# Optimization experiments

Measured on AMD Instinct MI355X. Metric: run time of the kernel, lower is better.

The kernel has to match this reference:

```python
import jax, jax.numpy as jnp
import numpy as np

B, N, F = 4, 4096, 32
NG = 14  # number of gate graph-convs in GCNLSTM_Cell with memory state


def setup_inputs() -> dict:
    key = jax.random.key(0)
    ks = jax.random.split(key, 7)
    x = jax.random.normal(ks[0], (B, N, F), jnp.float32)
    h = jax.random.normal(ks[1], (B, N, F), jnp.float32)
    c = jax.random.normal(ks[2], (B, N, F), jnp.float32)
    m = jax.random.normal(ks[3], (B, N, F), jnp.float32)
    # weighted dense adjacency, scaled so row sums are O(1)
    adj = jax.random.uniform(ks[4], (N, N), jnp.float32) / N
    # 14 WeightedGraphConv layers: Dense F -> 2F (single FeedForward layer, no relu)
    W = jax.random.normal(ks[5], (NG, F, 2 * F), jnp.float32) * (1.0 / np.sqrt(F))
    b = jnp.zeros((NG, 2 * F), jnp.float32)
    return {"x": x, "h": h, "c": c, "m": m, "adj": adj, "W": W, "b": b}


def _gcn(ax, W, b):
    # ax: [B,N,F] = adj @ state (precomputed); Dense to 2F then GLU split.
    z = ax @ W + b  # [B,N,2F]
    ls, rs = jnp.split(z, 2, axis=-1)
    return ls * jax.nn.sigmoid(rs)


def reference(x, h, c, m, adj, W, b):
    # shared graph aggregation for x and h (adj is the same for all gates)
    ax = jnp.einsum('nm,bmf->bnf', adj, x)  # [B,N,F]
    ah = jnp.einsum('nm,bmf->bnf', adj, h)

    fx = _gcn(ax, W[0], b[0]); fh = _gcn(ah, W[1], b[1])
    ix = _gcn(ax, W[2], b[2]); ih = _gcn(ah, W[3], b[3])
    cx = _gcn(ax, W[4], b[4]); ch = _gcn(ah, W[5], b[5])
    ox = _gcn(ax, W[6], b[6]); oh = _gcn(ah, W[7], b[7])

    f = jax.nn.sigmoid(fx + fh)
    i = jax.nn.sigmoid(ix + ih)
    o = jax.nn.sigmoid(ox + oh)
    c_new = f * c + i * jnp.tanh(cx + ch)
    h1 = o * jnp.tanh(c_new)

    # memory-state block (6 more graph convs on h1 and m)
    ah1 = jnp.einsum('nm,bmf->bnf', adj, h1)
    am = jnp.einsum('nm,bmf->bnf', adj, m)
    sa_ih = _gcn(ah1, W[8], b[8]);  sa_im = _gcn(am, W[9], b[9])
    sa_gh = _gcn(ah1, W[10], b[10]); sa_gm = _gcn(am, W[11], b[11])
    sa_oh = _gcn(ah1, W[12], b[12]); sa_om = _gcn(am, W[13], b[13])

    i2 = jax.nn.sigmoid(sa_ih + sa_im)
    g = jax.nn.sigmoid(sa_gh + sa_gm)
    o2 = jax.nn.sigmoid(sa_oh + sa_om)
    m_new = i2 * m + (1.0 - i2) * g
    h_new = m_new * o2
    return h_new, c_new, m_new
```

## Files before the change

### kernel.cpp

```cpp
#include <hip/hip_runtime.h>
#include <stdint.h>

typedef __attribute__((ext_vector_type(4))) float f32x4;
typedef __attribute__((ext_vector_type(8))) short s16x8;

#define BB 4
#define NN 4096
#define FF 32
#define BNF (BB*NN*FF)

typedef __attribute__((address_space(3))) void       as3_void;
typedef const __attribute__((address_space(1))) void as1_cvoid;

static __device__ __forceinline__ float bf2f(uint16_t u) {
    union { uint32_t i; float f; } v; v.i = ((uint32_t)u) << 16; return v.f;
}
static __device__ __forceinline__ uint16_t f2bf(float f) {
    union { float f; uint32_t i; } v; v.f = f;
    uint32_t r = v.i + 0x7FFFu + ((v.i >> 16) & 1u);
    return (uint16_t)(r >> 16);
}
static __device__ __forceinline__ float sig_acc(float x) { return 1.0f / (1.0f + expf(-x)); }

__global__ __launch_bounds__(256) void prep_kernel(
    const float* __restrict__ adj, uint16_t* __restrict__ adjb, int cvtN,
    const float* __restrict__ Wf, uint16_t* __restrict__ Wp,
    const float* __restrict__ x, const float* __restrict__ h,
    const float* __restrict__ m,
    uint16_t* __restrict__ P, uint16_t* __restrict__ P2)
{
    int bid = blockIdx.x;
    int t = threadIdx.x;

    if (bid < cvtN) {
        size_t i = ((size_t)bid * 256 + t) * 8;
        float4 v0 = *(const float4*)(adj + i);
        float4 v1 = *(const float4*)(adj + i + 4);
        union { uint4 u; uint16_t e[8]; } o;
        o.e[0] = f2bf(v0.x); o.e[1] = f2bf(v0.y); o.e[2] = f2bf(v0.z); o.e[3] = f2bf(v0.w);
        o.e[4] = f2bf(v1.x); o.e[5] = f2bf(v1.y); o.e[6] = f2bf(v1.z); o.e[7] = f2bf(v1.w);
        *(uint4*)(adjb + i) = o.u;
        return;
    }
    bid -= cvtN;

    if (bid < 112) {
        int idx = bid * 256 + t;
        int g   = idx >> 11;
        int k   = (idx >> 6) & 31;
        int col = idx & 63;
        uint16_t v = f2bf(Wf[idx]);
        int gp = g >> 1;
        int sl = ((g & 1) << 2) | (k >> 3);
        int ph = sl ^ (col & 7);
        Wp[((gp * 64 + col) * 64) + ph * 8 + (k & 7)] = v;
        return;
    }
    bid -= 112;

    const float* src; uint16_t* dst; int rowbase, b, n0;
    if (bid < 512) {
        int tensor = bid >> 8;
        src = tensor ? h : x; dst = P; rowbase = tensor * 128;
        b = (bid >> 6) & 3; n0 = (bid & 63) * 64;
    } else {
        int q = bid - 512;
        src = m; dst = P2; rowbase = 128;
        b = q >> 6; n0 = (q & 63) * 64;
    }
    __shared__ uint16_t tl[32][65];
    {
        int i = t >> 2, ch = t & 3;
        size_t idx = ((size_t)(b * NN + n0 + i)) * FF + ch * 8;
        float4 v0 = *(const float4*)(src + idx);
        float4 v1 = *(const float4*)(src + idx + 4);
        uint16_t e[8] = { f2bf(v0.x), f2bf(v0.y), f2bf(v0.z), f2bf(v0.w),
                          f2bf(v1.x), f2bf(v1.y), f2bf(v1.z), f2bf(v1.w) };
        #pragma unroll
        for (int k = 0; k < 8; k++) tl[ch * 8 + k][i] = e[k];
    }
    __syncthreads();
    {
        int f = t >> 3, ch = t & 7;
        union { uint4 u; uint16_t e[8]; } v;
        #pragma unroll
        for (int k = 0; k < 8; k++) v.e[k] = tl[f][ch * 8 + k];
        size_t row = (size_t)(rowbase + b * 32 + f);
        *(uint4*)(dst + row * NN + n0 + ch * 8) = v.u;
    }
}

__global__ __launch_bounds__(256) void gemm_kernel(
    const void* __restrict__ Av,
    const uint16_t* __restrict__ Bt,
    float* __restrict__ part, uint16_t* __restrict__ Cb,
    int kLen, int direct, int isf32A)
{
    int mt = blockIdx.x, nt = blockIdx.y, ks = blockIdx.z;
    int m0 = mt * 128, c0 = nt * 128, k0 = ks * kLen;
    __shared__ __align__(16) uint16_t aL[128 * 32];
    __shared__ __align__(16) uint16_t bL[128 * 32];
    int t = threadIdx.x;
    int lane = t & 63, w = t >> 6;
    int wm = (w & 1) * 64, wn = (w >> 1) * 64;
    int lm = lane & 15, lk = lane >> 4;

    const uint16_t* A16 = (const uint16_t*)Av;
    const float*    Af  = (const float*)Av;

    f32x4 acc[4][4] = {};

    for (int kk = k0; kk < k0 + kLen; kk += 32) {
        if (!isf32A) {
            #pragma unroll
            for (int q = 0; q < 2; q++) {
                int pos  = q * 4096 + t * 16;
                int row  = pos >> 6;
                int slot = ((pos >> 4) & 3) ^ ((row >> 1) & 3);
                int col  = slot * 8;
                size_t aidx = (size_t)(m0 + row) * 4096 + kk + col;
                size_t bidx = (size_t)(c0 + row) * 4096 + kk + col;
                __builtin_amdgcn_global_load_lds((as1_cvoid*)(A16 + aidx),
                                                 (as3_void*)((char*)aL + pos), 16, 0, 0);
                __builtin_amdgcn_global_load_lds((as1_cvoid*)(Bt + bidx),
                                                 (as3_void*)((char*)bL + pos), 16, 0, 0);
            }
        } else {
            union { uint4 u; uint16_t e[8]; } sa[2], sb[2];
            #pragma unroll
            for (int q = 0; q < 2; q++) {
                int pos  = q * 4096 + t * 16;
                int row  = pos >> 6;
                int slot = ((pos >> 4) & 3) ^ ((row >> 1) & 3);
                int col  = slot * 8;
                size_t aidx = (size_t)(m0 + row) * 4096 + kk + col;
                size_t bidx = (size_t)(c0 + row) * 4096 + kk + col;
                union { uint4 u[2]; float f[8]; } va;
                va.u[0] = *(const uint4*)(Af + aidx);
                va.u[1] = *(const uint4*)(Af + aidx + 4);
                #pragma unroll
                for (int k = 0; k < 8; k++) sa[q].e[k] = f2bf(va.f[k]);
                sb[q].u = *(const uint4*)(Bt + bidx);
            }
            #pragma unroll
            for (int q = 0; q < 2; q++) {
                int pos = q * 4096 + t * 16;
                *(uint4*)((char*)aL + pos) = sa[q].u;
                *(uint4*)((char*)bL + pos) = sb[q].u;
            }
        }
        __syncthreads();
        s16x8 af[4], bfr[4];
        #pragma unroll
        for (int i = 0; i < 4; i++) {
            int r = wm + i * 16 + lm;
            af[i] = *(const s16x8*)(aL + r * 32 + ((lk ^ ((r >> 1) & 3)) * 8));
        }
        #pragma unroll
        for (int j = 0; j < 4; j++) {
            int r = wn + j * 16 + lm;
            bfr[j] = *(const s16x8*)(bL + r * 32 + ((lk ^ ((r >> 1) & 3)) * 8));
        }
        #pragma unroll
        for (int i = 0; i < 4; i++)
            #pragma unroll
            for (int j = 0; j < 4; j++)
                acc[i][j] = __builtin_amdgcn_mfma_f32_16x16x32_bf16(af[i], bfr[j], acc[i][j], 0, 0, 0);
        __syncthreads();
    }

    int r4 = (lane >> 4) * 4;
    if (direct) {
        #pragma unroll
        for (int i = 0; i < 4; i++)
            #pragma unroll
            for (int j = 0; j < 4; j++) {
                int c = c0 + wn + j * 16 + lm;
                int mr = m0 + wm + i * 16 + r4;
                union { uint2 u; uint16_t e[4]; } v;
                #pragma unroll
                for (int r = 0; r < 4; r++) v.e[r] = f2bf(acc[i][j][r]);
                *(uint2*)(Cb + (size_t)c * 4096 + mr) = v.u;
            }
    } else {
        #pragma unroll
        for (int i = 0; i < 4; i++)
            #pragma unroll
            for (int j = 0; j < 4; j++) {
                int c = c0 + wn + j * 16 + lm;
                int mr = m0 + wm + i * 16 + r4;
                *(f32x4*)(part + ((size_t)ks * 256 + c) * 4096 + mr) = acc[i][j];
            }
    }
}

__global__ __launch_bounds__(256) void fuse1_kernel(
    const float* __restrict__ part,
    const uint16_t* __restrict__ Cbi,
    const uint16_t* __restrict__ Wp,
    const float* __restrict__ bf_,
    const float* __restrict__ cf,
    float* __restrict__ cnew, uint16_t* __restrict__ S2t, int ns)
{
    __shared__ float    AL[64 * 17];
    __shared__ float    SX[4][64][9];
    __shared__ uint16_t H1[32 * 18];

    int t = threadIdx.x;
    int bid = blockIdx.x;
    int b = bid >> 8, n0 = (bid & 255) * 16;
    int lane = t & 63, w = t >> 6;
    int j = lane & 15, kg = lane >> 4;
    int ej = t & 15, erow = (t >> 4) & 15;

    float cv[2];
    #pragma unroll
    for (int hh = 0; hh < 2; hh++)
        cv[hh] = cf[((size_t)(b * NN + n0 + erow)) * FF + ej + hh * 16];

    {
        int r = t >> 2, ch = t & 3;
        int crow = (r < 32) ? (b * 32 + r) : (128 + b * 32 + (r - 32));
        if (ns) {
            const float* gp = part + (size_t)crow * 4096 + n0 + ch * 4;
            f32x4 cur = *(const f32x4*)gp;
            f32x4 sum = {};
            for (int ks = 0; ks < ns; ks++) {
                f32x4 nxt;
                if (ks + 1 < ns) nxt = *(const f32x4*)(gp + (size_t)(ks + 1) * (256 * 4096));
                sum += cur;
                if (ks + 1 < ns) cur = nxt;
            }
            #pragma unroll
            for (int e = 0; e < 4; e++) AL[r * 17 + ch * 4 + e] = sum[e];
        } else {
            const uint16_t* cp = Cbi + (size_t)crow * 4096 + n0 + ch * 4;
            uint2 v = *(const uint2*)cp;
            const uint16_t* pe = (const uint16_t*)&v;
            #pragma unroll
            for (int e = 0; e < 4; e++) AL[r * 17 + ch * 4 + e] = bf2f(pe[e]);
        }
    }
    __syncthreads();

    s16x8 a_ax, a_ah;
    #pragma unroll
    for (int e = 0; e < 8; e++) {
        int k = kg * 8 + e;
        a_ax[e] = (short)f2bf(AL[k * 17 + j]);
        a_ah[e] = (short)f2bf(AL[(32 + k) * 17 + j]);
    }
    {
        int p = w;
        int g0 = p * 2, g1 = p * 2 + 1;
        f32x4 ac0[4] = {}, ac1[4] = {};
        #pragma unroll
        for (int ct = 0; ct < 4; ct++) {
            int col = ct * 16 + j;
            int ph0 = (kg)     ^ (col & 7);
            int ph1 = (4 + kg) ^ (col & 7);
            s16x8 b0 = *(const s16x8*)(Wp + (p * 64 + col) * 64 + ph0 * 8);
            s16x8 b1 = *(const s16x8*)(Wp + (p * 64 + col) * 64 + ph1 * 8);
            ac0[ct] = __builtin_amdgcn_mfma_f32_16x16x32_bf16(a_ax, b0, ac0[ct], 0, 0, 0);
            ac1[ct] = __builtin_amdgcn_mfma_f32_16x16x32_bf16(a_ah, b1, ac1[ct], 0, 0, 0);
        }
        #pragma unroll
        for (int hh = 0; hh < 2; hh++)
            #pragma unroll
            for (int r = 0; r < 4; r++) {
                float z0l = ac0[hh][r]     + bf_[g0 * 64 + hh * 16 + j];
                float z0r = ac0[2 + hh][r] + bf_[g0 * 64 + 32 + hh * 16 + j];
                float z1l = ac1[hh][r]     + bf_[g1 * 64 + hh * 16 + j];
                float z1r = ac1[2 + hh][r] + bf_[g1 * 64 + 32 + hh * 16 + j];
                SX[p][lane][hh * 4 + r] = z0l * sig_acc(z0r) + z1l * sig_acc(z1r);
            }
    }
    __syncthreads();

    {
        int pl = ((erow >> 2) << 4) | ej;
        int ridx = erow & 3;
        #pragma unroll
        for (int hh = 0; hh < 2; hh++) {
            float s0 = SX[0][pl][hh * 4 + ridx];
            float s1 = SX[1][pl][hh * 4 + ridx];
            float s2 = SX[2][pl][hh * 4 + ridx];
            float s3 = SX[3][pl][hh * 4 + ridx];
            float fg = sig_acc(s0), ig = sig_acc(s1);
            float cc = tanhf(s2),   og = sig_acc(s3);
            float cn = fg * cv[hh] + ig * cc;
            size_t gidx = ((size_t)(b * NN + n0 + erow)) * FF + ej + hh * 16;
            cnew[gidx] = cn;
            H1[(ej + hh * 16) * 18 + erow] = f2bf(og * tanhf(cn));
        }
    }
    __syncthreads();
    if (t < 64) {
        int f = t >> 1, half = t & 1;
        union { uint4 u; uint16_t e[8]; } v;
        #pragma unroll
        for (int k = 0; k < 8; k++) v.e[k] = H1[f * 18 + half * 8 + k];
        *(uint4*)(S2t + ((size_t)(b * 32 + f)) * NN + n0 + half * 8) = v.u;
    }
}

__global__ __launch_bounds__(256) void fuse2_kernel(
    const float* __restrict__ part,
    const uint16_t* __restrict__ Cbi,
    const uint16_t* __restrict__ Wp,
    const float* __restrict__ bf_,
    const float* __restrict__ mf,
    float* __restrict__ hnew, float* __restrict__ mnew, int ns)
{
    __shared__ float AL[64 * 17];
    __shared__ float SX[3][64][9];

    int t = threadIdx.x;
    int bid = blockIdx.x;
    int b = bid >> 8, n0 = (bid & 255) * 16;
    int lane = t & 63, w = t >> 6;
    int j = lane & 15, kg = lane >> 4;
    int ej = t & 15, erow = (t >> 4) & 15;

    float mv[2];
    #pragma unroll
    for (int hh = 0; hh < 2; hh++)
        mv[hh] = mf[((size_t)(b * NN + n0 + erow)) * FF + ej + hh * 16];

    {
        int r = t >> 2, ch = t & 3;
        int crow = (r < 32) ? (b * 32 + r) : (128 + b * 32 + (r - 32));
        if (ns) {
            const float* gp = part + (size_t)crow * 4096 + n0 + ch * 4;
            f32x4 cur = *(const f32x4*)gp;
            f32x4 sum = {};
            for (int ks = 0; ks < ns; ks++) {
                f32x4 nxt;
                if (ks + 1 < ns) nxt = *(const f32x4*)(gp + (size_t)(ks + 1) * (256 * 4096));
                sum += cur;
                if (ks + 1 < ns) cur = nxt;
            }
            #pragma unroll
            for (int e = 0; e < 4; e++) AL[r * 17 + ch * 4 + e] = sum[e];
        } else {
            const uint16_t* cp = Cbi + (size_t)crow * 4096 + n0 + ch * 4;
            uint2 v = *(const uint2*)cp;
            const uint16_t* pe = (const uint16_t*)&v;
            #pragma unroll
            for (int e = 0; e < 4; e++) AL[r * 17 + ch * 4 + e] = bf2f(pe[e]);
        }
    }
    __syncthreads();

    if (w < 3) {
        s16x8 a_h1, a_m;
        #pragma unroll
        for (int e = 0; e < 8; e++) {
            int k = kg * 8 + e;
            a_h1[e] = (short)f2bf(AL[k * 17 + j]);
            a_m[e]  = (short)f2bf(AL[(32 + k) * 17 + j]);
        }
        const uint16_t* WpG = Wp + 4 * 64 * 64;
        const float*    bG  = bf_ + 512;
        int p = w;
        int g0 = p * 2, g1 = p * 2 + 1;
        f32x4 ac0[4] = {}, ac1[4] = {};
        #pragma unroll
        for (int ct = 0; ct < 4; ct++) {
            int col = ct * 16 + j;
            int ph0 = (kg)     ^ (col & 7);
            int ph1 = (4 + kg) ^ (col & 7);
            s16x8 b0 = *(const s16x8*)(WpG + (p * 64 + col) * 64 + ph0 * 8);
            s16x8 b1 = *(const s16x8*)(WpG + (p * 64 + col) * 64 + ph1 * 8);
            ac0[ct] = __builtin_amdgcn_mfma_f32_16x16x32_bf16(a_h1, b0, ac0[ct], 0, 0, 0);
            ac1[ct] = __builtin_amdgcn_mfma_f32_16x16x32_bf16(a_m, b1, ac1[ct], 0, 0, 0);
        }
        #pragma unroll
        for (int hh = 0; hh < 2; hh++)
            #pragma unroll
            for (int r = 0; r < 4; r++) {
                float z0l = ac0[hh][r]     + bG[g0 * 64 + hh * 16 + j];
                float z0r = ac0[2 + hh][r] + bG[g0 * 64 + 32 + hh * 16 + j];
                float z1l = ac1[hh][r]     + bG[g1 * 64 + hh * 16 + j];
                float z1r = ac1[2 + hh][r] + bG[g1 * 64 + 32 + hh * 16 + j];
                SX[p][lane][hh * 4 + r] = z0l * sig_acc(z0r) + z1l * sig_acc(z1r);
            }
    }
    __syncthreads();

    {
        int pl = ((erow >> 2) << 4) | ej;
        int ridx = erow & 3;
        #pragma unroll
        for (int hh = 0; hh < 2; hh++) {
            float s0 = SX[0][pl][hh * 4 + ridx];
            float s1 = SX[1][pl][hh * 4 + ridx];
            float s2 = SX[2][pl][hh * 4 + ridx];
            float i2 = sig_acc(s0);
            float gg = sig_acc(s1);
            float o2 = sig_acc(s2);
            float mn = i2 * mv[hh] + (1.0f - i2) * gg;
            size_t gidx = ((size_t)(b * NN + n0 + erow)) * FF + ej + hh * 16;
            mnew[gidx] = mn;
            hnew[gidx] = mn * o2;
        }
    }
}

extern "C" void kernel_launch(void* const* d_in, const int* in_sizes, int n_in,
                              void* d_out, int out_size, void* d_ws, size_t ws_size,
                              hipStream_t stream) {
    (void)in_sizes; (void)n_in; (void)out_size;
    const float* x   = (const float*)d_in[0];
    const float* h   = (const float*)d_in[1];
    const float* c   = (const float*)d_in[2];
    const float* m   = (const float*)d_in[3];
    const float* adj = (const float*)d_in[4];
    const float* W   = (const float*)d_in[5];
    const float* bb  = (const float*)d_in[6];
    float* out = (float*)d_out;

    char* ws = (char*)d_ws;
    int haveAdjb = ws_size >= (size_t)(72u << 20);
    uint16_t* adjb = (uint16_t*)ws;
    size_t pOff = haveAdjb ? (size_t)(32u << 20) : 0;
    uint16_t* P    = (uint16_t*)(ws + pOff);
    uint16_t* P2   = (uint16_t*)(ws + pOff + (2u << 20));
    uint16_t* Cbuf = (uint16_t*)(ws + pOff + (4u << 20));
    uint16_t* Wp   = (uint16_t*)(ws + pOff + (6u << 20));
    size_t partOff = pOff + (7u << 20);
    float* part = (float*)(ws + partOff);

    if (ws_size < (8u << 20)) return;
    size_t avail = ws_size - partOff;
    int ns = 0;
    if      (avail >= (size_t)(32u << 20)) ns = 8;
    else if (avail >= (size_t)(16u << 20)) ns = 4;
    else if (avail >= (size_t)( 8u << 20)) ns = 2;
    else if (avail >= (size_t)( 4u << 20)) ns = 1;

    const void* Agemm = haveAdjb ? (const void*)adjb : (const void*)adj;
    int isf32A = haveAdjb ? 0 : 1;
    int cvtN = haveAdjb ? 8192 : 0;

    prep_kernel<<<cvtN + 112 + 768, 256, 0, stream>>>(adj, adjb, cvtN, W, Wp, x, h, m, P, P2);

    if (ns) {
        gemm_kernel<<<dim3(32, 2, ns), 256, 0, stream>>>(Agemm, P, part, nullptr, 4096 / ns, 0, isf32A);
    } else {
        gemm_kernel<<<dim3(32, 2, 1), 256, 0, stream>>>(Agemm, P, nullptr, Cbuf, 4096, 1, isf32A);
    }
    fuse1_kernel<<<1024, 256, 0, stream>>>(part, Cbuf, Wp, bb, c, out + BNF, P2, ns);
    if (ns) {
        gemm_kernel<<<dim3(32, 2, ns), 256, 0, stream>>>(Agemm, P2, part, nullptr, 4096 / ns, 0, isf32A);
    } else {
        gemm_kernel<<<dim3(32, 2, 1), 256, 0, stream>>>(Agemm, P2, nullptr, Cbuf, 4096, 1, isf32A);
    }
    fuse2_kernel<<<1024, 256, 0, stream>>>(part, Cbuf, Wp, bb, m, out, out + 2 * BNF, ns);
}
```

Before: 187.5 us.

## Replace split-K partial-sum GEMM with small-M-tile full-K GEMM writing bf16 directly

The adjacency GEMM used 128x128 tiles with split-K across up to 8 slices, writing fp32 partials that the fuse kernels then summed. It now uses 32x128 tiles over the full K range, launching 256 blocks, and writes bf16 output directly. This removes the partial-buffer write and read traffic and the reduction loop, and lowers the workspace needed to keep the bf16 adjacency copy. The cost is less data reuse per tile: the 128-wide B tile is reloaded by every M tile, and the full-K loop is serial per block.

```diff
diff --git a/kernel.cpp b/kernel.cpp
--- a/kernel.cpp
+++ b/kernel.cpp
@@ -93,114 +93,106 @@
 __global__ __launch_bounds__(256) void gemm_kernel(
     const void* __restrict__ Av,
     const uint16_t* __restrict__ Bt,
-    float* __restrict__ part, uint16_t* __restrict__ Cb,
-    int kLen, int direct, int isf32A)
+    uint16_t* __restrict__ Cb,
+    int isf32A)
 {
-    int mt = blockIdx.x, nt = blockIdx.y, ks = blockIdx.z;
-    int m0 = mt * 128, c0 = nt * 128, k0 = ks * kLen;
-    __shared__ __align__(16) uint16_t aL[128 * 32];
+    int nt = blockIdx.x, mt = blockIdx.y;
+    int m0 = mt * 32, c0 = nt * 128;
+    __shared__ __align__(16) uint16_t aL[32 * 32];
     __shared__ __align__(16) uint16_t bL[128 * 32];
     int t = threadIdx.x;
     int lane = t & 63, w = t >> 6;
-    int wm = (w & 1) * 64, wn = (w >> 1) * 64;
     int lm = lane & 15, lk = lane >> 4;
 
     const uint16_t* A16 = (const uint16_t*)Av;
     const float*    Af  = (const float*)Av;
 
-    f32x4 acc[4][4] = {};
-
-    for (int kk = k0; kk < k0 + kLen; kk += 32) {
+    f32x4 acc[2][2] = {};
+
+    for (int kk = 0; kk < 4096; kk += 32) {
         if (!isf32A) {
+            if (t < 128) {
+                int pos  = t * 16;
+                int row  = pos >> 6;
+                int slot = ((pos >> 4) & 3) ^ ((row >> 1) & 3);
+                size_t aidx = (size_t)(m0 + row) * 4096 + kk + slot * 8;
+                __builtin_amdgcn_global_load_lds((as1_cvoid*)(A16 + aidx),
+                                                 (as3_void*)((char*)aL + pos), 16, 0, 0);
+            }
             #pragma unroll
             for (int q = 0; q < 2; q++) {
                 int pos  = q * 4096 + t * 16;
                 int row  = pos >> 6;
                 int slot = ((pos >> 4) & 3) ^ ((row >> 1) & 3);
-                int col  = slot * 8;
-                size_t aidx = (size_t)(m0 + row) * 4096 + kk + col;
-                size_t bidx = (size_t)(c0 + row) * 4096 + kk + col;
-                __builtin_amdgcn_global_load_lds((as1_cvoid*)(A16 + aidx),
-                                                 (as3_void*)((char*)aL + pos), 16, 0, 0);
+                size_t bidx = (size_t)(c0 + row) * 4096 + kk + slot * 8;
                 __builtin_amdgcn_global_load_lds((as1_cvoid*)(Bt + bidx),
                                                  (as3_void*)((char*)bL + pos), 16, 0, 0);
             }
         } else {
-            union { uint4 u; uint16_t e[8]; } sa[2], sb[2];
+            union { uint4 u; uint16_t e[8]; } sa, sb[2];
+            int apos = t * 16, arow = apos >> 6;
+            if (t < 128) {
+                int slot = ((apos >> 4) & 3) ^ ((arow >> 1) & 3);
+                size_t aidx = (size_t)(m0 + arow) * 4096 + kk + slot * 8;
+                union { uint4 u[2]; float f[8]; } va;
+                va.u[0] = *(const uint4*)(Af + aidx);
+                va.u[1] = *(const uint4*)(Af + aidx + 4);
+                #pragma unroll
+                for (int k = 0; k < 8; k++) sa.e[k] = f2bf(va.f[k]);
+            }
             #pragma unroll
             for (int q = 0; q < 2; q++) {
                 int pos  = q * 4096 + t * 16;
                 int row  = pos >> 6;
                 int slot = ((pos >> 4) & 3) ^ ((row >> 1) & 3);
-                int col  = slot * 8;
-                size_t aidx = (size_t)(m0 + row) * 4096 + kk + col;
-                size_t bidx = (size_t)(c0 + row) * 4096 + kk + col;
-                union { uint4 u[2]; float f[8]; } va;
-                va.u[0] = *(const uint4*)(Af + aidx);
-                va.u[1] = *(const uint4*)(Af + aidx + 4);
-                #pragma unroll
-                for (int k = 0; k < 8; k++) sa[q].e[k] = f2bf(va.f[k]);
+                size_t bidx = (size_t)(c0 + row) * 4096 + kk + slot * 8;
                 sb[q].u = *(const uint4*)(Bt + bidx);
             }
-            #pragma unroll
-            for (int q = 0; q < 2; q++) {
-                int pos = q * 4096 + t * 16;
-                *(uint4*)((char*)aL + pos) = sa[q].u;
-                *(uint4*)((char*)bL + pos) = sb[q].u;
-            }
+            if (t < 128) *(uint4*)((char*)aL + apos) = sa.u;
+            #pragma unroll
+            for (int q = 0; q < 2; q++)
+                *(uint4*)((char*)bL + q * 4096 + t * 16) = sb[q].u;
         }
         __syncthreads();
-        s16x8 af[4], bfr[4];
-        #pragma unroll
-        for (int i = 0; i < 4; i++) {
-            int r = wm + i * 16 + lm;
+        s16x8 af[2], bfr[2];
+        #pragma unroll
+        for (int i = 0; i < 2; i++) {
+            int r = i * 16 + lm;
             af[i] = *(const s16x8*)(aL + r * 32 + ((lk ^ ((r >> 1) & 3)) * 8));
         }
         #pragma unroll
-        for (int j = 0; j < 4; j++) {
-            int r = wn + j * 16 + lm;
+        for (int j = 0; j < 2; j++) {
+            int r = w * 32 + j * 16 + lm;
             bfr[j] = *(const s16x8*)(bL + r * 32 + ((lk ^ ((r >> 1) & 3)) * 8));
         }
         #pragma unroll
-        for (int i = 0; i < 4; i++)
-            #pragma unroll
-            for (int j = 0; j < 4; j++)
+        for (int i = 0; i < 2; i++)
+            #pragma unroll
+            for (int j = 0; j < 2; j++)
                 acc[i][j] = __builtin_amdgcn_mfma_f32_16x16x32_bf16(af[i], bfr[j], acc[i][j], 0, 0, 0);
         __syncthreads();
     }
 
     int r4 = (lane >> 4) * 4;
-    if (direct) {
-        #pragma unroll
-        for (int i = 0; i < 4; i++)
-            #pragma unroll
-            for (int j = 0; j < 4; j++) {
-                int c = c0 + wn + j * 16 + lm;
-                int mr = m0 + wm + i * 16 + r4;
-                union { uint2 u; uint16_t e[4]; } v;
-                #pragma unroll
-                for (int r = 0; r < 4; r++) v.e[r] = f2bf(acc[i][j][r]);
-                *(uint2*)(Cb + (size_t)c * 4096 + mr) = v.u;
-            }
-    } else {
-        #pragma unroll
-        for (int i = 0; i < 4; i++)
-            #pragma unroll
-            for (int j = 0; j < 4; j++) {
-                int c = c0 + wn + j * 16 + lm;
-                int mr = m0 + wm + i * 16 + r4;
-                *(f32x4*)(part + ((size_t)ks * 256 + c) * 4096 + mr) = acc[i][j];
-            }
-    }
+    #pragma unroll
+    for (int i = 0; i < 2; i++)
+        #pragma unroll
+        for (int j = 0; j < 2; j++) {
+            int c = c0 + w * 32 + j * 16 + lm;
+            int mr = m0 + i * 16 + r4;
+            union { uint2 u; uint16_t e[4]; } v;
+            #pragma unroll
+            for (int r = 0; r < 4; r++) v.e[r] = f2bf(acc[i][j][r]);
+            *(uint2*)(Cb + (size_t)c * 4096 + mr) = v.u;
+        }
 }
 
 __global__ __launch_bounds__(256) void fuse1_kernel(
-    const float* __restrict__ part,
     const uint16_t* __restrict__ Cbi,
     const uint16_t* __restrict__ Wp,
     const float* __restrict__ bf_,
     const float* __restrict__ cf,
-    float* __restrict__ cnew, uint16_t* __restrict__ S2t, int ns)
+    float* __restrict__ cnew, uint16_t* __restrict__ S2t)
 {
     __shared__ float    AL[64 * 17];
     __shared__ float    SX[4][64][9];
@@ -221,25 +213,11 @@
     {
         int r = t >> 2, ch = t & 3;
         int crow = (r < 32) ? (b * 32 + r) : (128 + b * 32 + (r - 32));
-        if (ns) {
-            const float* gp = part + (size_t)crow * 4096 + n0 + ch * 4;
-            f32x4 cur = *(const f32x4*)gp;
-            f32x4 sum = {};
-            for (int ks = 0; ks < ns; ks++) {
-                f32x4 nxt;
-                if (ks + 1 < ns) nxt = *(const f32x4*)(gp + (size_t)(ks + 1) * (256 * 4096));
-                sum += cur;
-                if (ks + 1 < ns) cur = nxt;
-            }
-            #pragma unroll
-            for (int e = 0; e < 4; e++) AL[r * 17 + ch * 4 + e] = sum[e];
-        } else {
-            const uint16_t* cp = Cbi + (size_t)crow * 4096 + n0 + ch * 4;
-            uint2 v = *(const uint2*)cp;
-            const uint16_t* pe = (const uint16_t*)&v;
-            #pragma unroll
-            for (int e = 0; e < 4; e++) AL[r * 17 + ch * 4 + e] = bf2f(pe[e]);
-        }
+        const uint16_t* cp = Cbi + (size_t)crow * 4096 + n0 + ch * 4;
+        uint2 v = *(const uint2*)cp;
+        const uint16_t* pe = (const uint16_t*)&v;
+        #pragma unroll
+        for (int e = 0; e < 4; e++) AL[r * 17 + ch * 4 + e] = bf2f(pe[e]);
     }
     __syncthreads();
 
@@ -305,12 +283,11 @@
 }
 
 __global__ __launch_bounds__(256) void fuse2_kernel(
-    const float* __restrict__ part,
     const uint16_t* __restrict__ Cbi,
     const uint16_t* __restrict__ Wp,
     const float* __restrict__ bf_,
     const float* __restrict__ mf,
-    float* __restrict__ hnew, float* __restrict__ mnew, int ns)
+    float* __restrict__ hnew, float* __restrict__ mnew)
 {
     __shared__ float AL[64 * 17];
     __shared__ float SX[3][64][9];
@@ -330,25 +307,11 @@
     {
         int r = t >> 2, ch = t & 3;
         int crow = (r < 32) ? (b * 32 + r) : (128 + b * 32 + (r - 32));
-        if (ns) {
-            const float* gp = part + (size_t)crow * 4096 + n0 + ch * 4;
-            f32x4 cur = *(const f32x4*)gp;
-            f32x4 sum = {};
-            for (int ks = 0; ks < ns; ks++) {
-                f32x4 nxt;
-                if (ks + 1 < ns) nxt = *(const f32x4*)(gp + (size_t)(ks + 1) * (256 * 4096));
-                sum += cur;
-                if (ks + 1 < ns) cur = nxt;
-            }
-            #pragma unroll
-            for (int e = 0; e < 4; e++) AL[r * 17 + ch * 4 + e] = sum[e];
-        } else {
-            const uint16_t* cp = Cbi + (size_t)crow * 4096 + n0 + ch * 4;
-            uint2 v = *(const uint2*)cp;
-            const uint16_t* pe = (const uint16_t*)&v;
-            #pragma unroll
-            for (int e = 0; e < 4; e++) AL[r * 17 + ch * 4 + e] = bf2f(pe[e]);
-        }
+        const uint16_t* cp = Cbi + (size_t)crow * 4096 + n0 + ch * 4;
+        uint2 v = *(const uint2*)cp;
+        const uint16_t* pe = (const uint16_t*)&v;
+        #pragma unroll
+        for (int e = 0; e < 4; e++) AL[r * 17 + ch * 4 + e] = bf2f(pe[e]);
     }
     __syncthreads();
 
@@ -421,23 +384,15 @@
     float* out = (float*)d_out;
 
     char* ws = (char*)d_ws;
-    int haveAdjb = ws_size >= (size_t)(72u << 20);
+    int haveAdjb = ws_size >= (size_t)(40u << 20);
     uint16_t* adjb = (uint16_t*)ws;
     size_t pOff = haveAdjb ? (size_t)(32u << 20) : 0;
     uint16_t* P    = (uint16_t*)(ws + pOff);
     uint16_t* P2   = (uint16_t*)(ws + pOff + (2u << 20));
     uint16_t* Cbuf = (uint16_t*)(ws + pOff + (4u << 20));
     uint16_t* Wp   = (uint16_t*)(ws + pOff + (6u << 20));
-    size_t partOff = pOff + (7u << 20);
-    float* part = (float*)(ws + partOff);
 
     if (ws_size < (8u << 20)) return;
-    size_t avail = ws_size - partOff;
-    int ns = 0;
-    if      (avail >= (size_t)(32u << 20)) ns = 8;
-    else if (avail >= (size_t)(16u << 20)) ns = 4;
-    else if (avail >= (size_t)( 8u << 20)) ns = 2;
-    else if (avail >= (size_t)( 4u << 20)) ns = 1;
 
     const void* Agemm = haveAdjb ? (const void*)adjb : (const void*)adj;
     int isf32A = haveAdjb ? 0 : 1;
@@ -445,16 +400,8 @@
 
     prep_kernel<<<cvtN + 112 + 768, 256, 0, stream>>>(adj, adjb, cvtN, W, Wp, x, h, m, P, P2);
 
-    if (ns) {
-        gemm_kernel<<<dim3(32, 2, ns), 256, 0, stream>>>(Agemm, P, part, nullptr, 4096 / ns, 0, isf32A);
-    } else {
-        gemm_kernel<<<dim3(32, 2, 1), 256, 0, stream>>>(Agemm, P, nullptr, Cbuf, 4096, 1, isf32A);
-    }
-    fuse1_kernel<<<1024, 256, 0, stream>>>(part, Cbuf, Wp, bb, c, out + BNF, P2, ns);
-    if (ns) {
-        gemm_kernel<<<dim3(32, 2, ns), 256, 0, stream>>>(Agemm, P2, part, nullptr, 4096 / ns, 0, isf32A);
-    } else {
-        gemm_kernel<<<dim3(32, 2, 1), 256, 0, stream>>>(Agemm, P2, nullptr, Cbuf, 4096, 1, isf32A);
-    }
-    fuse2_kernel<<<1024, 256, 0, stream>>>(part, Cbuf, Wp, bb, m, out, out + 2 * BNF, ns);
-}
+    gemm_kernel<<<dim3(2, 128), 256, 0, stream>>>(Agemm, P, Cbuf, isf32A);
+    fuse1_kernel<<<1024, 256, 0, stream>>>(Cbuf, Wp, bb, c, out + BNF, P2);
+    gemm_kernel<<<dim3(2, 128), 256, 0, stream>>>(Agemm, P2, Cbuf, isf32A);
+    fuse2_kernel<<<1024, 256, 0, stream>>>(Cbuf, Wp, bb, m, out, out + 2 * BNF);
+}
```

After: 244.8 us. 1.31x slower.
